# Performance work log

Hardware: AMD Instinct MI355X
Metric: run time of the kernel (lower is better)

## Reference

```python
import jax, jax.numpy as jnp
import numpy as np

DIM = 640
HEADS = 8
HEAD_DIM = 80
CROSS = 768
FF_INNER = 4 * DIM  # 2560
EPS = 1e-5
SCALE = HEAD_DIM ** -0.5


def _ln(x, w, b):
    m = jnp.mean(x, axis=-1, keepdims=True)
    v = jnp.var(x, axis=-1, keepdims=True)
    return (x - m) * jax.lax.rsqrt(v + EPS) * w + b


def _split_heads(x):  # [B,S,D] -> [B,H,S,dh]
    B, S, D = x.shape
    return x.reshape(B, S, HEADS, D // HEADS).transpose(0, 2, 1, 3)


def _merge_heads(x):  # [B,H,S,dh] -> [B,S,D]
    B, H, S, dh = x.shape
    return x.transpose(0, 2, 1, 3).reshape(B, S, H * dh)


def _mha(q, k, v):
    # q:[B,S,D] k,v:[B,Skv,D]
    qh, kh, vh = _split_heads(q), _split_heads(k), _split_heads(v)
    scores = jnp.einsum('bhqd,bhkd->bhqk', qh, kh) * SCALE
    probs = jax.nn.softmax(scores, axis=-1)
    out = jnp.einsum('bhqk,bhkd->bhqd', probs, vh)
    return _merge_heads(out)


def _forward(hidden_states, encoder_hidden_states, video_length, p):
    BF, S, D = hidden_states.shape
    f = video_length
    b = BF // f

    # ---- attn1: sparse causal self-attention ----
    x = _ln(hidden_states, p['ln1_w'], p['ln1_b'])
    q = x @ p['q1']
    k = x @ p['k1']
    v = x @ p['v1']
    former = jnp.concatenate([jnp.zeros((1,), jnp.int32), jnp.arange(f - 1, dtype=jnp.int32)])
    def gather_kv(t):  # [BF,S,D] -> [BF,2S,D]
        t = t.reshape(b, f, S, D)
        first = jnp.broadcast_to(t[:, 0:1], (b, f, S, D))
        prev = t[:, former]
        return jnp.concatenate([first, prev], axis=2).reshape(BF, 2 * S, D)
    k = gather_kv(k)
    v = gather_kv(v)
    attn1 = _mha(q, k, v) @ p['o1_w'] + p['o1_b']
    hidden_states = attn1 + hidden_states

    # ---- attn2: cross attention to text ----
    x = _ln(hidden_states, p['ln2_w'], p['ln2_b'])
    q = x @ p['q2']
    k = encoder_hidden_states @ p['k2']
    v = encoder_hidden_states @ p['v2']
    attn2 = _mha(q, k, v) @ p['o2_w'] + p['o2_b']
    hidden_states = attn2 + hidden_states

    # ---- feed-forward (geglu) ----
    x = _ln(hidden_states, p['ln3_w'], p['ln3_b'])
    proj = x @ p['ff_w1'] + p['ff_b1']
    h, gate = jnp.split(proj, 2, axis=-1)
    ff = (h * jax.nn.gelu(gate)) @ p['ff_w2'] + p['ff_b2']
    return ff + hidden_states


def setup_inputs() -> dict:
    key = jax.random.key(0)
    ks = jax.random.split(key, 20)
    s = lambda i, shape, scale=0.02: jax.random.normal(ks[i], shape, jnp.float32) * scale
    inp = {
        'hidden_states': jax.random.normal(ks[0], (8, 1024, DIM), jnp.float32),
        'encoder_hidden_states': jax.random.normal(ks[1], (8, 77, CROSS), jnp.float32),
        'video_length': 8,
        'ln1_w': jnp.ones((DIM,)), 'ln1_b': jnp.zeros((DIM,)),
        'q1': s(2, (DIM, DIM)), 'k1': s(3, (DIM, DIM)), 'v1': s(4, (DIM, DIM)),
        'o1_w': s(5, (DIM, DIM)), 'o1_b': jnp.zeros((DIM,)),
        'ln2_w': jnp.ones((DIM,)), 'ln2_b': jnp.zeros((DIM,)),
        'q2': s(6, (DIM, DIM)), 'k2': s(7, (CROSS, DIM)), 'v2': s(8, (CROSS, DIM)),
        'o2_w': s(9, (DIM, DIM)), 'o2_b': jnp.zeros((DIM,)),
        'ln3_w': jnp.ones((DIM,)), 'ln3_b': jnp.zeros((DIM,)),
        'ff_w1': s(10, (DIM, 2 * FF_INNER)), 'ff_b1': jnp.zeros((2 * FF_INNER,)),
        'ff_w2': s(11, (FF_INNER, DIM)), 'ff_b2': jnp.zeros((DIM,)),
    }
    return inp


def reference(hidden_states, encoder_hidden_states, video_length,
              ln1_w, ln1_b, q1, k1, v1, o1_w, o1_b,
              ln2_w, ln2_b, q2, k2, v2, o2_w, o2_b,
              ln3_w, ln3_b, ff_w1, ff_b1, ff_w2, ff_b2):
    p = dict(ln1_w=ln1_w, ln1_b=ln1_b, q1=q1, k1=k1, v1=v1, o1_w=o1_w, o1_b=o1_b,
             ln2_w=ln2_w, ln2_b=ln2_b, q2=q2, k2=k2, v2=v2, o2_w=o2_w, o2_b=o2_b,
             ln3_w=ln3_w, ln3_b=ln3_b, ff_w1=ff_w1, ff_b1=ff_b1, ff_w2=ff_w2, ff_b2=ff_b2)
    return _forward(hidden_states, encoder_hidden_states, video_length, p)
```

## Files before the change

### kernel.cpp

```cpp
#include <hip/hip_runtime.h>
#include <stdint.h>

#define TOK   8192
#define DIM   640
#define HEADS 8
#define HD    80
#define SEQ   1024
#define CROSS 768
#define ETOK  616
#define FFI   2560
#define SCALE 0.11180339887498949f

typedef unsigned short u16;
typedef unsigned int   u32;

using bf8   = __attribute__((ext_vector_type(8))) short;
using f32x4 = __attribute__((ext_vector_type(4))) float;

struct __align__(16) U4 { u32 x, y, z, w; };
struct __align__(8)  U2 { u32 x, y; };

__device__ __forceinline__ float bf2f(u16 u){
  union { u32 i; float f; } v; v.i = ((u32)u) << 16; return v.f;
}
__device__ __forceinline__ u16 f2bf(float f){
  union { float f; u32 i; } v; v.f = f;
  u32 r = v.i + 0x7fffu + ((v.i >> 16) & 1u);
  return (u16)(r >> 16);
}
__device__ __forceinline__ u32 cvtpk_bf16(float lo, float hi){
  u32 r; asm("v_cvt_pk_bf16_f32 %0, %1, %2" : "=v"(r) : "v"(lo), "v"(hi)); return r;
}
__device__ __forceinline__ float gelu_t(float x){
  float y = 0.7978845608028654f * (x + 0.044715f * x * x * x);
  float e = __expf(2.f * y);
  return 0.5f * x * (2.f - 2.f / (e + 1.f));
}

__device__ __forceinline__ void gl2lds16(const u16* g, u16* l){
  __builtin_amdgcn_global_load_lds(
      (const __attribute__((address_space(1))) void*)g,
      (__attribute__((address_space(3))) void*)l, 16, 0, 0);
}

struct CvtJob  { const float* s; u16* d; int n; };
struct CvtJobs { CvtJob j[11]; };
__global__ __launch_bounds__(256) void cvt_all(CvtJobs jobs)
{
  const CvtJob jb = jobs.j[blockIdx.y];
  for (long i = (long)blockIdx.x*256 + threadIdx.x; i < jb.n; i += (long)gridDim.x*256)
    jb.d[i] = f2bf(jb.s[i]);
}

struct TJob  { const float* s; u16* d; int R, C, srcLd, dstLd; };
struct TJobs { TJob j[10]; };
__global__ __launch_bounds__(256) void transpose_tiled(TJobs jobs)
{
  const TJob jb = jobs.j[blockIdx.y];
  const int tilesC = jb.C >> 6;
  const int nt = (jb.R >> 6) * tilesC;
  if ((int)blockIdx.x >= nt) return;
  const int tr = (blockIdx.x / tilesC) << 6, tc = (blockIdx.x % tilesC) << 6;
  __shared__ u16 t[64][65];
  const int tid = threadIdx.x;
  const int rr = tid >> 3, c8 = (tid & 7) * 8;
  #pragma unroll
  for (int p = 0; p < 2; ++p){
    const int r = rr + p*32;
    const float* s = &jb.s[(long)(tr + r)*jb.srcLd + tc + c8];
    #pragma unroll
    for (int j = 0; j < 8; ++j) t[r][c8 + j] = f2bf(s[j]);
  }
  __syncthreads();
  #pragma unroll
  for (int p = 0; p < 2; ++p){
    const int c = rr + p*32;
    u16 tmp[8];
    #pragma unroll
    for (int j = 0; j < 8; ++j) tmp[j] = t[c8 + j][c];
    *(U4*)&jb.d[(long)(tc + c)*jb.dstLd + tr + c8] = *(U4*)tmp;
  }
}

__global__ __launch_bounds__(256) void transpose_tile(
    const u16* __restrict__ src, u16* __restrict__ dst,
    int srcLd, int dstLd)
{
  __shared__ u16 t[64][65];
  const int tr = blockIdx.y << 6, tc = blockIdx.x << 6;
  const int tid = threadIdx.x;
  const int rr = tid >> 3, c8 = (tid & 7) * 8;
  #pragma unroll
  for (int p = 0; p < 2; ++p){
    const int r = rr + p*32;
    U4 v = *(const U4*)&src[(long)(tr + r)*srcLd + tc + c8];
    const u16* pv = (const u16*)&v;
    #pragma unroll
    for (int j = 0; j < 8; ++j) t[r][c8 + j] = pv[j];
  }
  __syncthreads();
  #pragma unroll
  for (int p = 0; p < 2; ++p){
    const int c = rr + p*32;
    u16 tmp[8];
    #pragma unroll
    for (int j = 0; j < 8; ++j) tmp[j] = t[c8 + j][c];
    *(U4*)&dst[(long)(tc + c)*dstLd + tr + c8] = *(U4*)tmp;
  }
}

__global__ __launch_bounds__(256) void transpose_v2(
    const u16* __restrict__ src, u16* __restrict__ dst)
{
  int idx = blockIdx.x*256 + threadIdx.x;
  if (idx >= ETOK*DIM) return;
  int rr = idx / DIM, d = idx - rr*DIM;
  int g = rr / 77, j = rr - g*77;
  dst[(long)d*DIM + g*80 + j] = src[(long)rr*(2*DIM) + DIM + d];
}

__global__ __launch_bounds__(256) void ln_k(
    const void* __restrict__ src, const u16* __restrict__ w,
    const u16* __restrict__ b, u16* __restrict__ dst, int srcf32)
{
  __shared__ float xr[DIM];
  __shared__ float red[256];
  const int tid = threadIdx.x;
  const long row = blockIdx.x;
  float ls = 0.f;
  for (int i = tid; i < DIM; i += 256){
    float v = srcf32 ? ((const float*)src)[row*DIM + i]
                     : bf2f(((const u16*)src)[row*DIM + i]);
    xr[i] = v; ls += v;
  }
  red[tid] = ls; __syncthreads();
  for (int o = 128; o > 0; o >>= 1){ if (tid < o) red[tid] += red[tid+o]; __syncthreads(); }
  const float mean = red[0] * (1.f/DIM);
  __syncthreads();
  float lq = 0.f;
  for (int i = tid; i < DIM; i += 256){ float d = xr[i] - mean; lq += d*d; }
  red[tid] = lq; __syncthreads();
  for (int o = 128; o > 0; o >>= 1){ if (tid < o) red[tid] += red[tid+o]; __syncthreads(); }
  const float var = red[0] * (1.f/DIM);
  const float rs = rsqrtf(var + 1e-5f);
  u16* q = dst + row*DIM;
  for (int i = tid; i < DIM; i += 256)
    q[i] = f2bf((xr[i] - mean)*rs*bf2f(w[i]) + bf2f(b[i]));
}

template<int BN>
__global__ __launch_bounds__(256) void gemm_bt(
    const u16* __restrict__ A, const u16* __restrict__ BT, void* __restrict__ C,
    int M, int N, int K, int lda, int ldb, int ldc,
    const u16* __restrict__ bias, const void* __restrict__ res, int ldr,
    int resf32, int outf32)
{
  constexpr int NT  = BN/32;
  constexpr int BCH = BN/16;
  constexpr int BPW = BCH/4;
  __shared__ __align__(16) u16 sA[2][8*512];
  __shared__ __align__(16) u16 sB[2][BCH*512];
  const int tid  = threadIdx.x;
  const int wave = tid >> 6, lane = tid & 63;
  const int quad = lane >> 4, l16 = lane & 15;
  const int m0 = blockIdx.y * 128, n0 = blockIdx.x * BN;
  const int wm = (wave >> 1) * 64, wn = (wave & 1) * (BN/2);
  const int srow = lane & 15;
  const int scol = (lane >> 4) * 8;

  long aoff[2];
  #pragma unroll
  for (int i = 0; i < 2; ++i){
    int r = m0 + (wave*2 + i)*16 + srow;
    r = r < M ? r : M - 1;
    aoff[i] = (long)r*lda + scol;
  }
  long boff[BPW];
  #pragma unroll
  for (int i = 0; i < BPW; ++i){
    int r = n0 + (wave*BPW + i)*16 + srow;
    boff[i] = (long)r*ldb + scol;
  }

  f32x4 acc[4][NT] = {};
  #pragma unroll
  for (int i = 0; i < 2; ++i)   gl2lds16(&A[aoff[i]],  &sA[0][(wave*2 + i)*512]);
  #pragma unroll
  for (int i = 0; i < BPW; ++i) gl2lds16(&BT[boff[i]], &sB[0][(wave*BPW + i)*512]);
  __syncthreads();

  int cur = 0;
  for (int k0 = 0; ; ){
    const int kn = k0 + 32;
    if (kn < K){
      #pragma unroll
      for (int i = 0; i < 2; ++i)   gl2lds16(&A[aoff[i] + kn],  &sA[cur^1][(wave*2 + i)*512]);
      #pragma unroll
      for (int i = 0; i < BPW; ++i) gl2lds16(&BT[boff[i] + kn], &sB[cur^1][(wave*BPW + i)*512]);
    }
    bf8 a[4], b[NT];
    #pragma unroll
    for (int mt = 0; mt < 4; ++mt)  a[mt] = *(const bf8*)&sA[cur][((wm>>4) + mt)*512 + lane*8];
    #pragma unroll
    for (int nt = 0; nt < NT; ++nt) b[nt] = *(const bf8*)&sB[cur][((wn>>4) + nt)*512 + lane*8];
    #pragma unroll
    for (int mt = 0; mt < 4; ++mt)
      #pragma unroll
      for (int nt = 0; nt < NT; ++nt)
        acc[mt][nt] = __builtin_amdgcn_mfma_f32_16x16x32_bf16(a[mt], b[nt], acc[mt][nt], 0, 0, 0);
    k0 = kn;
    if (k0 >= K) break;
    __syncthreads();
    cur ^= 1;
  }
  #pragma unroll
  for (int mt = 0; mt < 4; ++mt){
    const int rl = wm + mt*16 + quad*4;
    #pragma unroll
    for (int nt = 0; nt < NT; ++nt){
      const int col = n0 + wn + nt*16 + l16;
      float bv = bias ? bf2f(bias[col]) : 0.f;
      #pragma unroll
      for (int r = 0; r < 4; ++r){
        int row = m0 + rl + r;
        if (row < M){
          float v = acc[mt][nt][r] + bv;
          if (res) v += resf32 ? ((const float*)res)[(long)row*ldr + col]
                               : bf2f(((const u16*)res)[(long)row*ldr + col]);
          if (outf32) ((float*)C)[(long)row*ldc + col] = v;
          else        ((u16*)C) [(long)row*ldc + col] = f2bf(v);
        }
      }
    }
  }
}

__global__ __launch_bounds__(256) void gemm_geglu(
    const u16* __restrict__ A, const u16* __restrict__ W, u16* __restrict__ C,
    const u16* __restrict__ bias)
{
  __shared__ __align__(16) u16 sA[2][8*512];
  __shared__ __align__(16) u16 sH[2][4*512];
  __shared__ __align__(16) u16 sG[2][4*512];
  const int tid  = threadIdx.x;
  const int wave = tid >> 6, lane = tid & 63;
  const int quad = lane >> 4, l16 = lane & 15;
  const int m0 = blockIdx.y * 128, n0 = blockIdx.x * 64;
  const int wm = (wave >> 1) * 64, wn = (wave & 1) * 32;
  const int srow = lane & 15;
  const int scol = (lane >> 4) * 8;

  long aoff[2];
  #pragma unroll
  for (int i = 0; i < 2; ++i)
    aoff[i] = (long)(m0 + (wave*2 + i)*16 + srow)*DIM + scol;
  const long hoff = (long)(n0 + wave*16 + srow)*DIM + scol;
  const long goff = (long)(FFI + n0 + wave*16 + srow)*DIM + scol;

  f32x4 ah[4][2] = {}, ag[4][2] = {};
  #pragma unroll
  for (int i = 0; i < 2; ++i) gl2lds16(&A[aoff[i]], &sA[0][(wave*2 + i)*512]);
  gl2lds16(&W[hoff], &sH[0][wave*512]);
  gl2lds16(&W[goff], &sG[0][wave*512]);
  __syncthreads();

  int cur = 0;
  for (int k0 = 0; ; ){
    const int kn = k0 + 32;
    if (kn < DIM){
      #pragma unroll
      for (int i = 0; i < 2; ++i) gl2lds16(&A[aoff[i] + kn], &sA[cur^1][(wave*2 + i)*512]);
      gl2lds16(&W[hoff + kn], &sH[cur^1][wave*512]);
      gl2lds16(&W[goff + kn], &sG[cur^1][wave*512]);
    }
    bf8 a[4];
    #pragma unroll
    for (int mt = 0; mt < 4; ++mt) a[mt] = *(const bf8*)&sA[cur][((wm>>4) + mt)*512 + lane*8];
    #pragma unroll
    for (int nt = 0; nt < 2; ++nt){
      bf8 bh = *(const bf8*)&sH[cur][((wn>>4) + nt)*512 + lane*8];
      bf8 bg = *(const bf8*)&sG[cur][((wn>>4) + nt)*512 + lane*8];
      #pragma unroll
      for (int mt = 0; mt < 4; ++mt){
        ah[mt][nt] = __builtin_amdgcn_mfma_f32_16x16x32_bf16(a[mt], bh, ah[mt][nt], 0, 0, 0);
        ag[mt][nt] = __builtin_amdgcn_mfma_f32_16x16x32_bf16(a[mt], bg, ag[mt][nt], 0, 0, 0);
      }
    }
    k0 = kn;
    if (k0 >= DIM) break;
    __syncthreads();
    cur ^= 1;
  }
  #pragma unroll
  for (int mt = 0; mt < 4; ++mt){
    const int rl = wm + mt*16 + quad*4;
    #pragma unroll
    for (int nt = 0; nt < 2; ++nt){
      const int col = n0 + wn + nt*16 + l16;
      const float bh = bf2f(bias[col]);
      const float bg = bf2f(bias[FFI + col]);
      #pragma unroll
      for (int r = 0; r < 4; ++r){
        int row = m0 + rl + r;
        float h = ah[mt][nt][r] + bh;
        float g = ag[mt][nt][r] + bg;
        C[(long)row*FFI + col] = f2bf(h * gelu_t(g));
      }
    }
  }
}

template<int MODE>
__global__ __launch_bounds__(256) void attn_k(
    const u16* __restrict__ qbuf, const u16* __restrict__ kbuf,
    const u16* __restrict__ vT, u16* __restrict__ out)
{
  constexpr int QLD  = MODE ? DIM      : 3*DIM;
  constexpr int KLD  = MODE ? 2*DIM    : 3*DIM;
  constexpr int KCOL = MODE ? 0        : DIM;
  constexpr int VLD  = MODE ? DIM      : TOK;
  constexpr int NK   = MODE ? 77       : 2*SEQ;
  constexpr int NCH  = MODE ? 3        : 64;
  constexpr float C1   = SCALE * 1.4426950408889634f;
  constexpr float THRR = 8.0f / C1;

  const int qt = blockIdx.x, h = blockIdx.y, g = blockIdx.z;
  const int tid = threadIdx.x, wave = tid >> 6, lane = tid & 63;
  const int quad = lane >> 4, l16 = lane & 15;

  __shared__ __align__(16) u16 Qs[64*104];
  __shared__ __align__(16) u16 Ks[32*104];
  __shared__ __align__(16) u16 Vs[80*40];
  __shared__ __align__(16) u16 Ps[4][16*40];

  const int qrow0 = g*SEQ + qt*64;
  for (int v = tid; v < 640; v += 256){
    int r = v/10, c8 = (v - r*10)*8;
    *(U4*)&Qs[r*104 + c8] = *(const U4*)&qbuf[(long)(qrow0 + r)*QLD + h*HD + c8];
  }
  for (int v = tid; v < 128; v += 256){
    U4 z = {0,0,0,0};
    *(U4*)&Qs[(v>>1)*104 + 80 + (v&1)*8] = z;
  }
  for (int v = tid; v < 64; v += 256){
    U4 z = {0,0,0,0};
    *(U4*)&Ks[(v>>1)*104 + 80 + (v&1)*8] = z;
  }

  const int kr0 = tid/10,        kc0 = (tid - kr0*10)*8;
  const int kr1 = (tid+256)/10,  kc1 = ((tid+256) - kr1*10)*8;
  const int vd0 = tid >> 2,      vk0 = (tid & 3)*8;
  const int vd1 = (tid+256) >> 2;
  const int former = (g == 0) ? 0 : (g - 1);

  auto krow_of = [&](int c)->int{
    if (MODE == 0){
      int kb = c*32;
      int fr = (kb >> 10) ? former : 0;
      return fr*SEQ + (kb & (SEQ-1));
    }
    return 0;
  };
  U4 kA, kB, vA, vB;
  auto load_regs = [&](int c){
    if (MODE == 0){
      int kro = krow_of(c);
      kA = *(const U4*)&kbuf[(long)(kro + kr0)*KLD + KCOL + h*HD + kc0];
      if (tid < 64) kB = *(const U4*)&kbuf[(long)(kro + kr1)*KLD + KCOL + h*HD + kc1];
      vA = *(const U4*)&vT[(long)(h*HD + vd0)*VLD + kro + vk0];
      if (tid < 64) vB = *(const U4*)&vT[(long)(h*HD + vd1)*VLD + kro + vk0];
    } else {
      int kb = c*32;
      int j0 = kb + kr0; j0 = j0 < NK ? j0 : NK-1;
      kA = *(const U4*)&kbuf[((long)g*77 + j0)*KLD + KCOL + h*HD + kc0];
      if (tid < 64){
        int j1 = kb + kr1; j1 = j1 < NK ? j1 : NK-1;
        kB = *(const U4*)&kbuf[((long)g*77 + j1)*KLD + KCOL + h*HD + kc1];
      }
      vA = *(const U4*)&vT[(long)(h*HD + vd0)*VLD + g*80 + kb + vk0];
      if (tid < 64) vB = *(const U4*)&vT[(long)(h*HD + vd1)*VLD + g*80 + kb + vk0];
    }
  };
  load_regs(0);
  __syncthreads();

  bf8 qf[3];
  #pragma unroll
  for (int ks = 0; ks < 3; ++ks)
    qf[ks] = *(const bf8*)&Qs[(wave*16 + l16)*104 + ks*32 + quad*8];

  f32x4 o[5] = {};
  float mrun = -1e30f, lrun = 0.f, nmc = 0.f;

  for (int c = 0; c < NCH; ++c){
    const int kbase = c*32;
    *(U4*)&Ks[kr0*104 + kc0] = kA;
    if (tid < 64) *(U4*)&Ks[kr1*104 + kc1] = kB;
    *(U4*)&Vs[vd0*40 + vk0] = vA;
    if (tid < 64) *(U4*)&Vs[vd1*40 + vk0] = vB;
    __syncthreads();
    if (MODE == 1 && kbase + 32 > NK){
      for (int v = tid; v < 80*32; v += 256){
        int d = v >> 5, cc = v & 31;
        if (kbase + cc >= NK) Vs[d*40 + cc] = 0;
      }
      __syncthreads();
    }
    if (c + 1 < NCH) load_regs(c + 1);

    f32x4 s0 = {}, s1 = {};
    __builtin_amdgcn_s_setprio(1);
    #pragma unroll
    for (int ks = 0; ks < 3; ++ks){
      bf8 kf0 = *(const bf8*)&Ks[l16*104        + ks*32 + quad*8];
      bf8 kf1 = *(const bf8*)&Ks[(16 + l16)*104 + ks*32 + quad*8];
      s0 = __builtin_amdgcn_mfma_f32_16x16x32_bf16(kf0, qf[ks], s0, 0, 0, 0);
      s1 = __builtin_amdgcn_mfma_f32_16x16x32_bf16(kf1, qf[ks], s1, 0, 0, 0);
    }
    __builtin_amdgcn_s_setprio(0);

    if (MODE == 1){
      const int kg = kbase + quad*4;
      #pragma unroll
      for (int r = 0; r < 4; ++r){
        if (kg + r >= NK)      s0[r] = -1e30f;
        if (kg + 16 + r >= NK) s1[r] = -1e30f;
      }
    }
    float mxs = fmaxf(fmaxf(fmaxf(s0[0],s0[1]), fmaxf(s0[2],s0[3])),
                      fmaxf(fmaxf(s1[0],s1[1]), fmaxf(s1[2],s1[3])));
    mxs = fmaxf(mxs, __shfl_xor(mxs, 16, 64));
    mxs = fmaxf(mxs, __shfl_xor(mxs, 32, 64));
    if (!__all(mxs - mrun <= THRR)){
      float mn = fmaxf(mrun, mxs);
      float al = exp2f((mrun - mn)*C1);
      mrun = mn; nmc = -mrun*C1;
      lrun *= al;
      float a0 = __shfl(al, quad*4 + 0, 16);
      float a1 = __shfl(al, quad*4 + 1, 16);
      float a2 = __shfl(al, quad*4 + 2, 16);
      float a3 = __shfl(al, quad*4 + 3, 16);
      #pragma unroll
      for (int dt = 0; dt < 5; ++dt){
        o[dt][0] *= a0; o[dt][1] *= a1; o[dt][2] *= a2; o[dt][3] *= a3;
      }
    }
    #pragma unroll
    for (int r = 0; r < 4; ++r){
      s0[r] = exp2f(__builtin_fmaf(s0[r], C1, nmc));
      s1[r] = exp2f(__builtin_fmaf(s1[r], C1, nmc));
    }
    float rs = ((s0[0]+s0[1])+(s0[2]+s0[3])) + ((s1[0]+s1[1])+(s1[2]+s1[3]));
    rs += __shfl_xor(rs, 16, 64);
    rs += __shfl_xor(rs, 32, 64);
    lrun += rs;

    U2 w01, w23;
    w01.x = cvtpk_bf16(s0[0], s0[1]);  w01.y = cvtpk_bf16(s0[2], s0[3]);
    w23.x = cvtpk_bf16(s1[0], s1[1]);  w23.y = cvtpk_bf16(s1[2], s1[3]);
    U2* pr = (U2*)&Ps[wave][l16*40];
    pr[quad]     = w01;
    pr[4 + quad] = w23;
    asm volatile("s_waitcnt lgkmcnt(0)" ::: "memory");
    bf8 pf = *(const bf8*)&Ps[wave][l16*40 + quad*8];
    __builtin_amdgcn_s_setprio(1);
    #pragma unroll
    for (int dt = 0; dt < 5; ++dt){
      bf8 vf = *(const bf8*)&Vs[(dt*16 + l16)*40 + quad*8];
      o[dt] = __builtin_amdgcn_mfma_f32_16x16x32_bf16(pf, vf, o[dt], 0, 0, 0);
    }
    __builtin_amdgcn_s_setprio(0);
    __syncthreads();
  }

  float linv[4];
  #pragma unroll
  for (int r = 0; r < 4; ++r)
    linv[r] = __builtin_amdgcn_rcpf(__shfl(lrun, quad*4 + r, 16));
  const int orow0 = qrow0 + wave*16 + quad*4;
  #pragma unroll
  for (int dt = 0; dt < 5; ++dt){
    const int col = h*HD + dt*16 + l16;
    #pragma unroll
    for (int r = 0; r < 4; ++r)
      out[(long)(orow0 + r)*DIM + col] = f2bf(o[dt][r] * linv[r]);
  }
}

extern "C" void kernel_launch(void* const* d_in, const int* in_sizes, int n_in,
                              void* d_out, int out_size, void* d_ws, size_t ws_size,
                              hipStream_t stream)
{
  const float* hidden = (const float*)d_in[0];
  const float* enc    = (const float*)d_in[1];
  const float* ln1w = (const float*)d_in[3],  *ln1b = (const float*)d_in[4];
  const float* q1   = (const float*)d_in[5],  *k1   = (const float*)d_in[6];
  const float* v1   = (const float*)d_in[7],  *o1w  = (const float*)d_in[8];
  const float* o1b  = (const float*)d_in[9];
  const float* ln2w = (const float*)d_in[10], *ln2b = (const float*)d_in[11];
  const float* q2   = (const float*)d_in[12], *k2   = (const float*)d_in[13];
  const float* v2   = (const float*)d_in[14], *o2w  = (const float*)d_in[15];
  const float* o2b  = (const float*)d_in[16];
  const float* ln3w = (const float*)d_in[17], *ln3b = (const float*)d_in[18];
  const float* fw1  = (const float*)d_in[19], *fb1  = (const float*)d_in[20];
  const float* fw2  = (const float*)d_in[21], *fb2  = (const float*)d_in[22];

  u16* ws = (u16*)d_ws;
  u16* Wqkv1T = ws;
  u16* o1T    = Wqkv1T + 1920*640;
  u16* q2T    = o1T    + 640*640;
  u16* Wkv2T  = q2T    + 640*640;
  u16* o2T    = Wkv2T  + 1280*768;
  u16* W1T    = o2T    + 640*640;
  u16* W2T    = W1T    + 5120*640;
  u16* xbuf   = W2T    + 640*2560;
  u16* qkv1   = xbuf   + (size_t)TOK*DIM;
  u16* v1T    = qkv1   + (size_t)TOK*3*DIM;
  u16* ffin   = qkv1;
  u16* attnb  = v1T    + (size_t)DIM*TOK;
  u16* hid2   = attnb  + (size_t)TOK*DIM;
  u16* hid3   = hid2   + (size_t)TOK*DIM;
  u16* q2buf  = hid3   + (size_t)TOK*DIM;
  u16* kv2    = q2buf  + (size_t)TOK*DIM;
  u16* v2T    = kv2    + (size_t)ETOK*2*DIM;
  u16* encm   = v2T    + 640*640 + 64;
  u16* bln1w  = encm   + (size_t)ETOK*CROSS;
  u16* bln1b  = bln1w + DIM;
  u16* bo1b   = bln1b + DIM;
  u16* bln2w  = bo1b  + DIM;
  u16* bln2b  = bln2w + DIM;
  u16* bo2b   = bln2b + DIM;
  u16* bln3w  = bo2b  + DIM;
  u16* bln3b  = bln3w + DIM;
  u16* bfb2   = bln3b + DIM;
  u16* bfb1   = bfb2  + DIM;
  u16* wsend  = bfb1  + 2*FFI;
  const size_t needed = ((size_t)(wsend - ws) + 64) * 2;
  if (ws_size < needed) return;

  dim3 blk(256);
  CvtJobs jobs;
  jobs.j[0]  = { enc,  encm,  ETOK*CROSS };
  jobs.j[1]  = { ln1w, bln1w, DIM };
  jobs.j[2]  = { ln1b, bln1b, DIM };
  jobs.j[3]  = { o1b,  bo1b,  DIM };
  jobs.j[4]  = { ln2w, bln2w, DIM };
  jobs.j[5]  = { ln2b, bln2b, DIM };
  jobs.j[6]  = { o2b,  bo2b,  DIM };
  jobs.j[7]  = { ln3w, bln3w, DIM };
  jobs.j[8]  = { ln3b, bln3b, DIM };
  jobs.j[9]  = { fb2,  bfb2,  DIM };
  jobs.j[10] = { fb1,  bfb1,  2*FFI };
  cvt_all<<<dim3(64,11), blk, 0, stream>>>(jobs);

  TJobs tj;
  tj.j[0] = { q1,  Wqkv1T,            640, 640,  640,  640 };
  tj.j[1] = { k1,  Wqkv1T + 640*640,  640, 640,  640,  640 };
  tj.j[2] = { v1,  Wqkv1T + 1280*640, 640, 640,  640,  640 };
  tj.j[3] = { o1w, o1T,               640, 640,  640,  640 };
  tj.j[4] = { q2,  q2T,               640, 640,  640,  640 };
  tj.j[5] = { k2,  Wkv2T,             768, 640,  640,  768 };
  tj.j[6] = { v2,  Wkv2T + 640*768,   768, 640,  640,  768 };
  tj.j[7] = { o2w, o2T,               640, 640,  640,  640 };
  tj.j[8] = { fw1, W1T,               640, 5120, 5120, 640 };
  tj.j[9] = { fw2, W2T,               2560,640,  640,  2560 };
  transpose_tiled<<<dim3(800,10), blk, 0, stream>>>(tj);

  ln_k<<<TOK, blk, 0, stream>>>(hidden, bln1w, bln1b, xbuf, 1);
  gemm_bt<128><<<dim3(15,64), blk, 0, stream>>>(xbuf, Wqkv1T, qkv1,
      TOK, 3*DIM, DIM, DIM, DIM, 3*DIM, nullptr, nullptr, 0, 0, 0);
  transpose_tile<<<dim3(10,128), blk, 0, stream>>>(qkv1 + 2*DIM, v1T, 3*DIM, TOK);
  attn_k<0><<<dim3(16,8,8), blk, 0, stream>>>(qkv1, qkv1, v1T, attnb);
  gemm_bt<64><<<dim3(10,64), blk, 0, stream>>>(attnb, o1T, hid2,
      TOK, DIM, DIM, DIM, DIM, DIM, bo1b, hidden, DIM, 1, 0);

  ln_k<<<TOK, blk, 0, stream>>>(hid2, bln2w, bln2b, xbuf, 0);
  gemm_bt<64><<<dim3(10,64), blk, 0, stream>>>(xbuf, q2T, q2buf,
      TOK, DIM, DIM, DIM, DIM, DIM, nullptr, nullptr, 0, 0, 0);
  gemm_bt<64><<<dim3(20,5), blk, 0, stream>>>(encm, Wkv2T, kv2,
      ETOK, 2*DIM, CROSS, CROSS, CROSS, 2*DIM, nullptr, nullptr, 0, 0, 0);
  transpose_v2<<<dim3((ETOK*DIM + 255)/256), blk, 0, stream>>>(kv2, v2T);
  attn_k<1><<<dim3(16,8,8), blk, 0, stream>>>(q2buf, kv2, v2T, attnb);
  gemm_bt<64><<<dim3(10,64), blk, 0, stream>>>(attnb, o2T, hid3,
      TOK, DIM, DIM, DIM, DIM, DIM, bo2b, hid2, DIM, 0, 0);

  ln_k<<<TOK, blk, 0, stream>>>(hid3, bln3w, bln3b, xbuf, 0);
  gemm_geglu<<<dim3(40,64), blk, 0, stream>>>(xbuf, W1T, ffin, bfb1);
  gemm_bt<64><<<dim3(10,64), blk, 0, stream>>>(ffin, W2T, d_out,
      TOK, DIM, FFI, FFI, FFI, DIM, bfb2, hid3, DIM, 0, 1);
}
```

Measured before the change: 790.3 us.

## Stage attention K/V tiles directly to LDS via global_load_lds in fragment layout

Replaces register-staged K/V loads in the attention kernel with global_load_lds direct-to-LDS copies, laid out so each lane reads its MFMA fragment contiguously. Padding and out-of-range keys now come from a small zeroed global block, and the cross-attention V transpose writes padded zeros itself, so the in-kernel zero-fill pass goes away. The old software prefetch is dropped: each chunk now issues its loads and waits on vmcnt(0) before computing, which may expose more memory latency.

```diff
diff --git a/kernel.cpp b/kernel.cpp
--- a/kernel.cpp
+++ b/kernel.cpp
@@ -43,6 +43,8 @@
       (__attribute__((address_space(3))) void*)l, 16, 0, 0);
 }
 
+__global__ void zero_k(u16* p){ p[threadIdx.x] = 0; }
+
 struct CvtJob  { const float* s; u16* d; int n; };
 struct CvtJobs { CvtJob j[11]; };
 __global__ __launch_bounds__(256) void cvt_all(CvtJobs jobs)
@@ -113,10 +115,12 @@
     const u16* __restrict__ src, u16* __restrict__ dst)
 {
   int idx = blockIdx.x*256 + threadIdx.x;
-  if (idx >= ETOK*DIM) return;
-  int rr = idx / DIM, d = idx - rr*DIM;
-  int g = rr / 77, j = rr - g*77;
-  dst[(long)d*DIM + g*80 + j] = src[(long)rr*(2*DIM) + DIM + d];
+  if (idx >= DIM*640) return;
+  int d = idx / 640, c = idx - d*640;
+  int g = c / 80, j = c - g*80;
+  u16 v = 0;
+  if (j < 77) v = src[(long)(g*77 + j)*(2*DIM) + DIM + d];
+  dst[(long)d*640 + c] = v;
 }
 
 __global__ __launch_bounds__(256) void ln_k(
@@ -313,7 +317,8 @@
 template<int MODE>
 __global__ __launch_bounds__(256) void attn_k(
     const u16* __restrict__ qbuf, const u16* __restrict__ kbuf,
-    const u16* __restrict__ vT, u16* __restrict__ out)
+    const u16* __restrict__ vT, u16* __restrict__ out,
+    const u16* __restrict__ zblk)
 {
   constexpr int QLD  = MODE ? DIM      : 3*DIM;
   constexpr int KLD  = MODE ? 2*DIM    : 3*DIM;
@@ -329,8 +334,8 @@
   const int quad = lane >> 4, l16 = lane & 15;
 
   __shared__ __align__(16) u16 Qs[64*104];
-  __shared__ __align__(16) u16 Ks[32*104];
-  __shared__ __align__(16) u16 Vs[80*40];
+  __shared__ __align__(16) u16 Kb[6*512];
+  __shared__ __align__(16) u16 Vb[5*512];
   __shared__ __align__(16) u16 Ps[4][16*40];
 
   const int qrow0 = g*SEQ + qt*64;
@@ -342,83 +347,76 @@
     U4 z = {0,0,0,0};
     *(U4*)&Qs[(v>>1)*104 + 80 + (v&1)*8] = z;
   }
-  for (int v = tid; v < 64; v += 256){
-    U4 z = {0,0,0,0};
-    *(U4*)&Ks[(v>>1)*104 + 80 + (v&1)*8] = z;
-  }
-
-  const int kr0 = tid/10,        kc0 = (tid - kr0*10)*8;
-  const int kr1 = (tid+256)/10,  kc1 = ((tid+256) - kr1*10)*8;
-  const int vd0 = tid >> 2,      vk0 = (tid & 3)*8;
-  const int vd1 = (tid+256) >> 2;
+  __syncthreads();
+
+  bf8 qf[3];
+  #pragma unroll
+  for (int ks = 0; ks < 3; ++ks)
+    qf[ks] = *(const bf8*)&Qs[(wave*16 + l16)*104 + ks*32 + quad*8];
+
   const int former = (g == 0) ? 0 : (g - 1);
 
-  auto krow_of = [&](int c)->int{
+  auto stage = [&](int c){
+    int krow0, vrow0;
     if (MODE == 0){
       int kb = c*32;
       int fr = (kb >> 10) ? former : 0;
-      return fr*SEQ + (kb & (SEQ-1));
-    }
-    return 0;
+      krow0 = fr*SEQ + (kb & (SEQ-1));
+      vrow0 = krow0;
+    } else {
+      krow0 = c*32;
+      vrow0 = g*80 + c*32;
+    }
+    #pragma unroll
+    for (int ci = 0; ci < 6; ++ci){
+      if ((ci & 3) == wave){
+        const int ck = ci / 3, ks = ci % 3;
+        const int d  = ks*32 + quad*8;
+        const int rl = ck*16 + l16;
+        const u16* src;
+        if (MODE == 0){
+          src = (d < HD) ? &kbuf[(long)(krow0 + rl)*KLD + KCOL + h*HD + d] : zblk;
+        } else {
+          int j = krow0 + rl; j = j < NK ? j : NK-1;
+          src = (d < HD) ? &kbuf[((long)g*77 + j)*KLD + KCOL + h*HD + d] : zblk;
+        }
+        gl2lds16(src, &Kb[ci*512]);
+      }
+    }
+    #pragma unroll
+    for (int vi = 0; vi < 5; ++vi){
+      if (((vi + 2) & 3) == wave){
+        const int dd = vi*16 + l16;
+        const u16* src;
+        if (MODE == 0){
+          src = &vT[(long)(h*HD + dd)*VLD + vrow0 + quad*8];
+        } else {
+          int key = c*32 + quad*8;
+          src = (key < 80) ? &vT[(long)(h*HD + dd)*VLD + vrow0 + quad*8] : zblk;
+        }
+        gl2lds16(src, &Vb[vi*512]);
+      }
+    }
   };
-  U4 kA, kB, vA, vB;
-  auto load_regs = [&](int c){
-    if (MODE == 0){
-      int kro = krow_of(c);
-      kA = *(const U4*)&kbuf[(long)(kro + kr0)*KLD + KCOL + h*HD + kc0];
-      if (tid < 64) kB = *(const U4*)&kbuf[(long)(kro + kr1)*KLD + KCOL + h*HD + kc1];
-      vA = *(const U4*)&vT[(long)(h*HD + vd0)*VLD + kro + vk0];
-      if (tid < 64) vB = *(const U4*)&vT[(long)(h*HD + vd1)*VLD + kro + vk0];
-    } else {
-      int kb = c*32;
-      int j0 = kb + kr0; j0 = j0 < NK ? j0 : NK-1;
-      kA = *(const U4*)&kbuf[((long)g*77 + j0)*KLD + KCOL + h*HD + kc0];
-      if (tid < 64){
-        int j1 = kb + kr1; j1 = j1 < NK ? j1 : NK-1;
-        kB = *(const U4*)&kbuf[((long)g*77 + j1)*KLD + KCOL + h*HD + kc1];
-      }
-      vA = *(const U4*)&vT[(long)(h*HD + vd0)*VLD + g*80 + kb + vk0];
-      if (tid < 64) vB = *(const U4*)&vT[(long)(h*HD + vd1)*VLD + g*80 + kb + vk0];
-    }
-  };
-  load_regs(0);
-  __syncthreads();
-
-  bf8 qf[3];
-  #pragma unroll
-  for (int ks = 0; ks < 3; ++ks)
-    qf[ks] = *(const bf8*)&Qs[(wave*16 + l16)*104 + ks*32 + quad*8];
 
   f32x4 o[5] = {};
   float mrun = -1e30f, lrun = 0.f, nmc = 0.f;
 
   for (int c = 0; c < NCH; ++c){
-    const int kbase = c*32;
-    *(U4*)&Ks[kr0*104 + kc0] = kA;
-    if (tid < 64) *(U4*)&Ks[kr1*104 + kc1] = kB;
-    *(U4*)&Vs[vd0*40 + vk0] = vA;
-    if (tid < 64) *(U4*)&Vs[vd1*40 + vk0] = vB;
+    stage(c);
+    asm volatile("s_waitcnt vmcnt(0)" ::: "memory");
     __syncthreads();
-    if (MODE == 1 && kbase + 32 > NK){
-      for (int v = tid; v < 80*32; v += 256){
-        int d = v >> 5, cc = v & 31;
-        if (kbase + cc >= NK) Vs[d*40 + cc] = 0;
-      }
-      __syncthreads();
-    }
-    if (c + 1 < NCH) load_regs(c + 1);
 
     f32x4 s0 = {}, s1 = {};
-    __builtin_amdgcn_s_setprio(1);
     #pragma unroll
     for (int ks = 0; ks < 3; ++ks){
-      bf8 kf0 = *(const bf8*)&Ks[l16*104        + ks*32 + quad*8];
-      bf8 kf1 = *(const bf8*)&Ks[(16 + l16)*104 + ks*32 + quad*8];
+      bf8 kf0 = *(const bf8*)&Kb[ks*512     + lane*8];
+      bf8 kf1 = *(const bf8*)&Kb[(3+ks)*512 + lane*8];
       s0 = __builtin_amdgcn_mfma_f32_16x16x32_bf16(kf0, qf[ks], s0, 0, 0, 0);
       s1 = __builtin_amdgcn_mfma_f32_16x16x32_bf16(kf1, qf[ks], s1, 0, 0, 0);
     }
-    __builtin_amdgcn_s_setprio(0);
-
+
+    const int kbase = c*32;
     if (MODE == 1){
       const int kg = kbase + quad*4;
       #pragma unroll
@@ -462,14 +460,13 @@
     pr[quad]     = w01;
     pr[4 + quad] = w23;
     asm volatile("s_waitcnt lgkmcnt(0)" ::: "memory");
+    __builtin_amdgcn_sched_barrier(0);
     bf8 pf = *(const bf8*)&Ps[wave][l16*40 + quad*8];
-    __builtin_amdgcn_s_setprio(1);
     #pragma unroll
     for (int dt = 0; dt < 5; ++dt){
-      bf8 vf = *(const bf8*)&Vs[(dt*16 + l16)*40 + quad*8];
+      bf8 vf = *(const bf8*)&Vb[dt*512 + lane*8];
       o[dt] = __builtin_amdgcn_mfma_f32_16x16x32_bf16(pf, vf, o[dt], 0, 0, 0);
     }
-    __builtin_amdgcn_s_setprio(0);
     __syncthreads();
   }
 
@@ -534,11 +531,14 @@
   u16* bln3b  = bln3w + DIM;
   u16* bfb2   = bln3b + DIM;
   u16* bfb1   = bfb2  + DIM;
-  u16* wsend  = bfb1  + 2*FFI;
+  u16* zblk   = bfb1  + 2*FFI;
+  u16* wsend  = zblk  + 64;
   const size_t needed = ((size_t)(wsend - ws) + 64) * 2;
   if (ws_size < needed) return;
 
   dim3 blk(256);
+  zero_k<<<1, 64, 0, stream>>>(zblk);
+
   CvtJobs jobs;
   jobs.j[0]  = { enc,  encm,  ETOK*CROSS };
   jobs.j[1]  = { ln1w, bln1w, DIM };
@@ -570,7 +570,7 @@
   gemm_bt<128><<<dim3(15,64), blk, 0, stream>>>(xbuf, Wqkv1T, qkv1,
       TOK, 3*DIM, DIM, DIM, DIM, 3*DIM, nullptr, nullptr, 0, 0, 0);
   transpose_tile<<<dim3(10,128), blk, 0, stream>>>(qkv1 + 2*DIM, v1T, 3*DIM, TOK);
-  attn_k<0><<<dim3(16,8,8), blk, 0, stream>>>(qkv1, qkv1, v1T, attnb);
+  attn_k<0><<<dim3(16,8,8), blk, 0, stream>>>(qkv1, qkv1, v1T, attnb, zblk);
   gemm_bt<64><<<dim3(10,64), blk, 0, stream>>>(attnb, o1T, hid2,
       TOK, DIM, DIM, DIM, DIM, DIM, bo1b, hidden, DIM, 1, 0);
 
@@ -579,8 +579,8 @@
       TOK, DIM, DIM, DIM, DIM, DIM, nullptr, nullptr, 0, 0, 0);
   gemm_bt<64><<<dim3(20,5), blk, 0, stream>>>(encm, Wkv2T, kv2,
       ETOK, 2*DIM, CROSS, CROSS, CROSS, 2*DIM, nullptr, nullptr, 0, 0, 0);
-  transpose_v2<<<dim3((ETOK*DIM + 255)/256), blk, 0, stream>>>(kv2, v2T);
-  attn_k<1><<<dim3(16,8,8), blk, 0, stream>>>(q2buf, kv2, v2T, attnb);
+  transpose_v2<<<dim3((DIM*640 + 255)/256), blk, 0, stream>>>(kv2, v2T);
+  attn_k<1><<<dim3(16,8,8), blk, 0, stream>>>(q2buf, kv2, v2T, attnb, zblk);
   gemm_bt<64><<<dim3(10,64), blk, 0, stream>>>(attnb, o2T, hid3,
       TOK, DIM, DIM, DIM, DIM, DIM, bo2b, hid2, DIM, 0, 0);
 
```

New measurement: 726.3 us. 1.09x faster.
